# Performance work log

Hardware: AMD Instinct MI355X
Metric: run time of the kernel (lower is better)

The kernel has to match this reference:

```python
import jax, jax.numpy as jnp
import numpy as np

EPS = 1e-5

def setup_inputs() -> dict:
    key = jax.random.key(0)
    k1, k2, k3, k4, k5 = jax.random.split(key, 5)
    B, C, H, W = 4, 256, 256, 256  # W == C == input_features (LayerNorm over last dim)
    O = 256  # output_features
    x = jax.random.normal(k1, (B, C, H, W), dtype=jnp.float32)
    y = jax.random.normal(k2, (B, C, H, W), dtype=jnp.float32)
    ln_weight = jax.random.normal(k3, (W,), dtype=jnp.float32) * 0.02 + 1.0
    ln_bias = jax.random.normal(k4, (W,), dtype=jnp.float32) * 0.02
    conv_weight = jax.random.normal(k5, (O, C), dtype=jnp.float32) * (1.0 / np.sqrt(C))  # 1x1 conv, no bias
    return {"x": x, "y": y, "ln_weight": ln_weight, "ln_bias": ln_bias, "conv_weight": conv_weight}


def reference(x, y, ln_weight, ln_bias, conv_weight):
    # residual add
    out = x + y  # [B, C, H, W]
    # LayerNorm over the last dim (W), matching nn.LayerNorm(normalized_shape=input_features)
    mean = jnp.mean(out, axis=-1, keepdims=True)
    var = jnp.mean(jnp.square(out - mean), axis=-1, keepdims=True)
    normed = (out - mean) * jax.lax.rsqrt(var + EPS) * ln_weight + ln_bias
    # 1x1 Conv2d (per-pixel matmul over channels), bias=False
    conv = jnp.einsum("bchw,oc->bohw", normed, conv_weight)
    # ReLU
    return jnp.maximum(conv, 0.0)
```

## Files before the change

### kernel.cpp

```cpp
#include <hip/hip_runtime.h>

typedef __bf16 bf16x8 __attribute__((ext_vector_type(8)));
typedef float floatx4 __attribute__((ext_vector_type(4)));

__device__ __forceinline__ unsigned short f2bf(float f) {
    unsigned int u = __builtin_bit_cast(unsigned int, f);
    u += 0x7fffu + ((u >> 16) & 1u);
    return (unsigned short)(u >> 16);
}

__global__ __launch_bounds__(256) void prep_kernel(const float* __restrict__ cw,
                                                   unsigned short* __restrict__ cwb,
                                                   float* __restrict__ S) {
    int o = blockIdx.x;
    int c = threadIdx.x;
    float w = cw[o * 256 + c];
    cwb[o * 256 + c] = f2bf(w);
    float s = w;
    #pragma unroll
    for (int off = 32; off; off >>= 1) s += __shfl_xor(s, off);
    __shared__ float ps[4];
    if ((c & 63) == 0) ps[c >> 6] = s;
    __syncthreads();
    if (c == 0) S[o] = ps[0] + ps[1] + ps[2] + ps[3];
}

__global__ __launch_bounds__(1024) void fused_kernel(const float* __restrict__ x,
                                                     const float* __restrict__ y,
                                                     const float* __restrict__ lnw,
                                                     const float* __restrict__ lnb,
                                                     const unsigned short* __restrict__ cwb,
                                                     const float* __restrict__ S,
                                                     float* __restrict__ out) {
    __shared__ unsigned short zt[256 * 256];

    int b = blockIdx.x >> 8;
    int h = blockIdx.x & 255;
    int t = threadIdx.x;
    int wave = t >> 6;
    int lane = t & 63;
    size_t plane = ((size_t)b << 24) + ((size_t)h << 8);

    float lw[4];
    #pragma unroll
    for (int j = 0; j < 4; ++j) lw[j] = lnw[lane + 64 * j];

    #pragma unroll
    for (int g = 0; g < 2; ++g) {
        int c0 = wave * 16 + g * 8;
        unsigned short fr[4][8];
        #pragma unroll
        for (int r = 0; r < 8; ++r) {
            int c = c0 + r;
            const float* xp = x + plane + ((size_t)c << 16);
            const float* yp = y + plane + ((size_t)c << 16);
            float z[4];
            float s = 0.0f, q = 0.0f;
            #pragma unroll
            for (int j = 0; j < 4; ++j) {
                float xv = xp[lane + 64 * j];
                float yv = yp[lane + 64 * j];
                z[j] = xv + yv;
                s += z[j];
                q += z[j] * z[j];
            }
            #pragma unroll
            for (int off = 32; off; off >>= 1) {
                s += __shfl_xor(s, off);
                q += __shfl_xor(q, off);
            }
            float mean = s * (1.0f / 256.0f);
            float rstd = rsqrtf(q * (1.0f / 256.0f) - mean * mean + 1e-5f);
            #pragma unroll
            for (int j = 0; j < 4; ++j) fr[j][r] = f2bf((z[j] - mean) * rstd * lw[j]);
        }
        int chunk = wave * 2 + g;
        int chunkp = chunk ^ (lane & 7);
        #pragma unroll
        for (int j = 0; j < 4; ++j) {
            int w = lane + 64 * j;
            uint4 v;
            v.x = (unsigned int)fr[j][0] | ((unsigned int)fr[j][1] << 16);
            v.y = (unsigned int)fr[j][2] | ((unsigned int)fr[j][3] << 16);
            v.z = (unsigned int)fr[j][4] | ((unsigned int)fr[j][5] << 16);
            v.w = (unsigned int)fr[j][6] | ((unsigned int)fr[j][7] << 16);
            *(uint4*)&zt[w * 256 + chunkp * 8] = v;
        }
    }
    __syncthreads();

    int llo = lane & 15;
    int lhi = lane >> 4;
    int o_base = (wave & 3) * 64;
    int p0 = (wave >> 2) * 64;
    float* ob = out + plane;

    floatx4 acc[4][4];
    #pragma unroll
    for (int u = 0; u < 4; ++u)
        #pragma unroll
        for (int s2 = 0; s2 < 4; ++s2)
            #pragma unroll
            for (int r = 0; r < 4; ++r) acc[u][s2][r] = 0.0f;

    #pragma unroll
    for (int kt = 0; kt < 8; ++kt) {
        bf16x8 bfrag[4], afrag[4];
        #pragma unroll
        for (int s2 = 0; s2 < 4; ++s2) {
            int w = p0 + 16 * s2 + llo;
            int chunkp = (kt * 4 + lhi) ^ (llo & 7);
            bfrag[s2] = *(const bf16x8*)&zt[w * 256 + chunkp * 8];
        }
        #pragma unroll
        for (int u = 0; u < 4; ++u)
            afrag[u] = *(const bf16x8*)(cwb + (size_t)(o_base + 16 * u + llo) * 256 + kt * 32 + lhi * 8);
        #pragma unroll
        for (int u = 0; u < 4; ++u)
            #pragma unroll
            for (int s2 = 0; s2 < 4; ++s2)
                acc[u][s2] = __builtin_amdgcn_mfma_f32_16x16x32_bf16(afrag[u], bfrag[s2], acc[u][s2], 0, 0, 0);
    }

    float lnbv[4];
    #pragma unroll
    for (int s2 = 0; s2 < 4; ++s2) lnbv[s2] = lnb[p0 + 16 * s2 + llo];
    #pragma unroll
    for (int u = 0; u < 4; ++u) {
        #pragma unroll
        for (int r = 0; r < 4; ++r) {
            int o = o_base + 16 * u + 4 * lhi + r;
            float so = S[o];
            #pragma unroll
            for (int s2 = 0; s2 < 4; ++s2) {
                float v = acc[u][s2][r] + so * lnbv[s2];
                v = v > 0.0f ? v : 0.0f;
                ob[((size_t)o << 16) + p0 + 16 * s2 + llo] = v;
            }
        }
    }
}

extern "C" void kernel_launch(void* const* d_in, const int* in_sizes, int n_in,
                              void* d_out, int out_size, void* d_ws, size_t ws_size,
                              hipStream_t stream) {
    const float* x   = (const float*)d_in[0];
    const float* y   = (const float*)d_in[1];
    const float* lnw = (const float*)d_in[2];
    const float* lnb = (const float*)d_in[3];
    const float* cw  = (const float*)d_in[4];
    float* out = (float*)d_out;

    unsigned short* cwb = (unsigned short*)d_ws;
    float* S            = (float*)((char*)d_ws + 131072);

    prep_kernel<<<256, 256, 0, stream>>>(cw, cwb, S);
    fused_kernel<<<1024, 1024, 0, stream>>>(x, y, lnw, lnb, cwb, S, out);
}
```

Baseline: 643.5 us.

## Split each plane across two blocks to halve LDS and raise occupancy

Each (b,h) plane is now handled by two 512-thread blocks, each owning half of the W positions for the GEMM and storing only its half of the normalized tile in LDS (64KB instead of 128KB). Each block still reads full rows to compute LayerNorm statistics, so input reads are duplicated. Block IDs are interleaved so the two halves of a plane run close in time and can hit in L2. The aim is more resident blocks per CU and better latency hiding, at the cost of redundant loads and reductions.

```diff
diff --git a/kernel.cpp b/kernel.cpp
--- a/kernel.cpp
+++ b/kernel.cpp
@@ -25,30 +25,33 @@
     if (c == 0) S[o] = ps[0] + ps[1] + ps[2] + ps[3];
 }
 
-__global__ __launch_bounds__(1024) void fused_kernel(const float* __restrict__ x,
-                                                     const float* __restrict__ y,
-                                                     const float* __restrict__ lnw,
-                                                     const float* __restrict__ lnb,
-                                                     const unsigned short* __restrict__ cwb,
-                                                     const float* __restrict__ S,
-                                                     float* __restrict__ out) {
-    __shared__ unsigned short zt[256 * 256];
+__global__ __launch_bounds__(512, 4) void fused_kernel(const float* __restrict__ x,
+                                                       const float* __restrict__ y,
+                                                       const float* __restrict__ lnw,
+                                                       const float* __restrict__ lnb,
+                                                       const unsigned short* __restrict__ cwb,
+                                                       const float* __restrict__ S,
+                                                       float* __restrict__ out) {
+    __shared__ unsigned short zt[128 * 256];
 
-    int b = blockIdx.x >> 8;
-    int h = blockIdx.x & 255;
+    int bid = blockIdx.x;
+    int plane_id = ((bid >> 4) << 3) | (bid & 7);
+    int hw = (bid >> 3) & 1;
+    int b = plane_id >> 8;
+    int h = plane_id & 255;
     int t = threadIdx.x;
     int wave = t >> 6;
     int lane = t & 63;
     size_t plane = ((size_t)b << 24) + ((size_t)h << 8);
 
-    float lw[4];
+    float lw[2];
     #pragma unroll
-    for (int j = 0; j < 4; ++j) lw[j] = lnw[lane + 64 * j];
+    for (int jl = 0; jl < 2; ++jl) lw[jl] = lnw[lane + 64 * (2 * hw + jl)];
 
     #pragma unroll
-    for (int g = 0; g < 2; ++g) {
-        int c0 = wave * 16 + g * 8;
-        unsigned short fr[4][8];
+    for (int g = 0; g < 4; ++g) {
+        int c0 = wave * 32 + g * 8;
+        unsigned short fr[2][8];
         #pragma unroll
         for (int r = 0; r < 8; ++r) {
             int c = c0 + r;
@@ -72,19 +75,20 @@
             float mean = s * (1.0f / 256.0f);
             float rstd = rsqrtf(q * (1.0f / 256.0f) - mean * mean + 1e-5f);
             #pragma unroll
-            for (int j = 0; j < 4; ++j) fr[j][r] = f2bf((z[j] - mean) * rstd * lw[j]);
+            for (int jl = 0; jl < 2; ++jl)
+                fr[jl][r] = f2bf((z[2 * hw + jl] - mean) * rstd * lw[jl]);
         }
-        int chunk = wave * 2 + g;
+        int chunk = wave * 4 + g;
         int chunkp = chunk ^ (lane & 7);
         #pragma unroll
-        for (int j = 0; j < 4; ++j) {
-            int w = lane + 64 * j;
+        for (int jl = 0; jl < 2; ++jl) {
+            int wl = lane + 64 * jl;
             uint4 v;
-            v.x = (unsigned int)fr[j][0] | ((unsigned int)fr[j][1] << 16);
-            v.y = (unsigned int)fr[j][2] | ((unsigned int)fr[j][3] << 16);
-            v.z = (unsigned int)fr[j][4] | ((unsigned int)fr[j][5] << 16);
-            v.w = (unsigned int)fr[j][6] | ((unsigned int)fr[j][7] << 16);
-            *(uint4*)&zt[w * 256 + chunkp * 8] = v;
+            v.x = (unsigned int)fr[jl][0] | ((unsigned int)fr[jl][1] << 16);
+            v.y = (unsigned int)fr[jl][2] | ((unsigned int)fr[jl][3] << 16);
+            v.z = (unsigned int)fr[jl][4] | ((unsigned int)fr[jl][5] << 16);
+            v.w = (unsigned int)fr[jl][6] | ((unsigned int)fr[jl][7] << 16);
+            *(uint4*)&zt[wl * 256 + chunkp * 8] = v;
         }
     }
     __syncthreads();
@@ -93,7 +97,7 @@
     int lhi = lane >> 4;
     int o_base = (wave & 3) * 64;
     int p0 = (wave >> 2) * 64;
-    float* ob = out + plane;
+    float* ob = out + plane + hw * 128;
 
     floatx4 acc[4][4];
     #pragma unroll
@@ -108,9 +112,9 @@
         bf16x8 bfrag[4], afrag[4];
         #pragma unroll
         for (int s2 = 0; s2 < 4; ++s2) {
-            int w = p0 + 16 * s2 + llo;
+            int wl = p0 + 16 * s2 + llo;
             int chunkp = (kt * 4 + lhi) ^ (llo & 7);
-            bfrag[s2] = *(const bf16x8*)&zt[w * 256 + chunkp * 8];
+            bfrag[s2] = *(const bf16x8*)&zt[wl * 256 + chunkp * 8];
         }
         #pragma unroll
         for (int u = 0; u < 4; ++u)
@@ -124,7 +128,7 @@
 
     float lnbv[4];
     #pragma unroll
-    for (int s2 = 0; s2 < 4; ++s2) lnbv[s2] = lnb[p0 + 16 * s2 + llo];
+    for (int s2 = 0; s2 < 4; ++s2) lnbv[s2] = lnb[hw * 128 + p0 + 16 * s2 + llo];
     #pragma unroll
     for (int u = 0; u < 4; ++u) {
         #pragma unroll
@@ -155,5 +159,5 @@
     float* S            = (float*)((char*)d_ws + 131072);
 
     prep_kernel<<<256, 256, 0, stream>>>(cw, cwb, S);
-    fused_kernel<<<1024, 1024, 0, stream>>>(x, y, lnw, lnb, cwb, S, out);
+    fused_kernel<<<2048, 512, 0, stream>>>(x, y, lnw, lnb, cwb, S, out);
 }
```

Result: no change. 652.5 us (+1.4%).
